# Optimization experiments

Measured on AMD Instinct MI355X. Metric: run time of the kernel, lower is better.

Reference implementation:

```python
import jax, jax.numpy as jnp
import numpy as np

N_NODES = 50000
N_EDGES = 800000
N_FEAT, N_HID, N_CLASS = 128, 128, 64


def _sage_conv(x, src, dst, Wl, Wr, b, n_nodes):
    # PyG SAGEConv (mean aggr): out = lin_l(mean_j x_j) + lin_r(x_i)
    msg = x[src]                                            # [E, d] gather
    agg = jax.ops.segment_sum(msg, dst, num_segments=n_nodes)
    deg = jax.ops.segment_sum(jnp.ones_like(dst, dtype=x.dtype), dst,
                              num_segments=n_nodes)
    agg = agg / jnp.maximum(deg, 1.0)[:, None]              # mean over in-neighbors
    return agg @ Wl + x @ Wr + b


def setup_inputs() -> dict:
    key = jax.random.key(0)
    ks = jax.random.split(key, 12)
    x = jax.random.normal(ks[0], (N_NODES, N_FEAT), dtype=jnp.float32)
    edge_index = jax.random.randint(ks[1], (2, N_EDGES), 0, N_NODES, dtype=jnp.int32)

    def glorot(k, fan_in, fan_out):
        s = jnp.sqrt(2.0 / (fan_in + fan_out)).astype(jnp.float32)
        return jax.random.normal(k, (fan_in, fan_out), dtype=jnp.float32) * s

    return {
        "x": x,
        "edge_index": edge_index,
        # layer 0: n_feat -> n_hid
        "Wl0": glorot(ks[2], N_FEAT, N_HID),
        "Wr0": glorot(ks[3], N_FEAT, N_HID),
        "b0": jnp.zeros((N_HID,), dtype=jnp.float32),
        # layer 1 (mid): n_hid -> n_hid
        "Wl1": glorot(ks[4], N_HID, N_HID),
        "Wr1": glorot(ks[5], N_HID, N_HID),
        "b1": jnp.zeros((N_HID,), dtype=jnp.float32),
        # layer 2 (out): n_hid -> n_class
        "Wl2": glorot(ks[6], N_HID, N_CLASS),
        "Wr2": glorot(ks[7], N_HID, N_CLASS),
        "b2": jnp.zeros((N_CLASS,), dtype=jnp.float32),
    }


def reference(x, edge_index, Wl0, Wr0, b0, Wl1, Wr1, b1, Wl2, Wr2, b2):
    src, dst = edge_index[0], edge_index[1]
    n = x.shape[0]
    # in_conv -> relu -> dropout(eval: identity)
    h = jax.nn.relu(_sage_conv(x, src, dst, Wl0, Wr0, b0, n))
    # mid_conv -> relu -> dropout(eval: identity)
    h = jax.nn.relu(_sage_conv(h, src, dst, Wl1, Wr1, b1, n))
    # out_conv (no relu/dropout)
    return _sage_conv(h, src, dst, Wl2, Wr2, b2, n)
```

## Files before the change

kernel.cpp:

```cpp
#include <hip/hip_runtime.h>

#define NFEAT 128
#define RS 128

using bf16x8 = __attribute__((ext_vector_type(8))) short;
using f32x4  = __attribute__((ext_vector_type(4))) float;
using f32x2  = __attribute__((ext_vector_type(2))) float;

__device__ __forceinline__ float bf2f(unsigned short u) {
    union { unsigned int i; float f; } v; v.i = ((unsigned int)u) << 16; return v.f;
}
__device__ __forceinline__ float bfhi2f(unsigned int hi16) {
    union { unsigned int i; float f; } v; v.i = hi16; return v.f;
}
__device__ __forceinline__ unsigned short f2bf(float f) {
    union { float f; unsigned int i; } v; v.f = f;
    unsigned int i = v.i;
    return (unsigned short)((i + 0x7FFFu + ((i >> 16) & 1u)) >> 16);
}
__device__ __forceinline__ unsigned int f4_to_fp8x4(float f0, float f1, float f2, float f3) {
    int p = __builtin_amdgcn_cvt_pk_fp8_f32(f0, f1, 0, false);
    p     = __builtin_amdgcn_cvt_pk_fp8_f32(f2, f3, p, true);
    return (unsigned int)p;
}


__global__ void zero_kernel(int* __restrict__ p, int n) {
    int i = blockIdx.x * 256 + threadIdx.x;
    if (i < n) p[i] = 0;
}

__global__ void hist_kernel(const int* __restrict__ dst, int* __restrict__ cnt,
                            int nE, int sliceN) {
    const int slice = blockIdx.x & 7;
    const int lo = slice * sliceN, hi = lo + sliceN;
    const int nb = gridDim.x >> 3;
    const int bs = blockIdx.x >> 3;
    for (int i = bs * 256 + threadIdx.x; i < nE; i += nb * 256) {
        int d = dst[i];
        if (d >= lo && d < hi) atomicAdd(&cnt[d], 1);
    }
}

__global__ void fill_kernel(const int* __restrict__ src, const int* __restrict__ dst,
                            int* __restrict__ cnt, int* __restrict__ col_idx,
                            int nE, int sliceN) {
    const int slice = blockIdx.x & 7;
    const int lo = slice * sliceN, hi = lo + sliceN;
    const int nb = gridDim.x >> 3;
    const int bs = blockIdx.x >> 3;
    for (int i = bs * 256 + threadIdx.x; i < nE; i += nb * 256) {
        int d = dst[i];
        int s = src[i];
        if (d >= lo && d < hi) {
            int pos = atomicAdd(&cnt[d], 1);
            col_idx[pos] = s;
        }
    }
}

__global__ void blocksum_kernel(const int* __restrict__ cnt, int* __restrict__ blockSum, int n) {
    int i = blockIdx.x * 256 + threadIdx.x;
    int d = (i < n) ? cnt[i] : 0;
    int lane = threadIdx.x & 63, wid = threadIdx.x >> 6;
    __shared__ int ws[4];
    int v = d;
    for (int off = 32; off; off >>= 1) v += __shfl_down(v, off);
    if (lane == 0) ws[wid] = v;
    __syncthreads();
    if (threadIdx.x == 0) blockSum[blockIdx.x] = ws[0] + ws[1] + ws[2] + ws[3];
}

__global__ void scan_write_kernel(int* __restrict__ cnt, const int* __restrict__ blockSum,
                                  int* __restrict__ row_ptr, float* __restrict__ inv_deg,
                                  int n) {
    const int b = blockIdx.x, tid = threadIdx.x;
    const int lane = tid & 63, wid = tid >> 6;
    __shared__ int wsA[4];
    __shared__ int wsB[4];
    int v = (tid < b) ? blockSum[tid] : 0;
    for (int off = 32; off; off >>= 1) v += __shfl_down(v, off);
    if (lane == 0) wsA[wid] = v;
    int i = b * 256 + tid;
    int d = (i < n) ? cnt[i] : 0;
    int s = d;
    for (int off = 1; off < 64; off <<= 1) {
        int t = __shfl_up(s, off);
        if (lane >= off) s += t;
    }
    if (lane == 63) wsB[wid] = s;
    __syncthreads();
    int blockOff = wsA[0] + wsA[1] + wsA[2] + wsA[3];
    int wOff = 0;
    for (int w = 0; w < wid; ++w) wOff += wsB[w];
    int excl = blockOff + wOff + s - d;
    if (i < n) {
        row_ptr[i] = excl;
        cnt[i]     = excl;
        inv_deg[i] = 1.0f / (float)(d > 1 ? d : 1);
    }
    if (i == n) row_ptr[n] = excl;
}


__global__ void xconv_kernel(const float* __restrict__ x, unsigned short* __restrict__ xc,
                             unsigned char* __restrict__ xq, int n) {
    int i = blockIdx.x * 256 + threadIdx.x;
    if (i >= n * 32) return;
    int node = i >> 5, fb = (i & 31) * 4;
    float4 v = *(const float4*)(x + (size_t)node * NFEAT + fb);
    uint2 hw;
    hw.x = (unsigned int)f2bf(v.x) | ((unsigned int)f2bf(v.y) << 16);
    hw.y = (unsigned int)f2bf(v.z) | ((unsigned int)f2bf(v.w) << 16);
    *(uint2*)(xc + (size_t)node * RS + fb) = hw;
    *(unsigned int*)(xq + (size_t)node * NFEAT + fb) = f4_to_fp8x4(v.x, v.y, v.z, v.w);
}

__global__ void wconv_all_kernel(const float* __restrict__ Wl0, const float* __restrict__ Wr0,
                                 const float* __restrict__ Wl1, const float* __restrict__ Wr1,
                                 const float* __restrict__ Wl2, const float* __restrict__ Wr2,
                                 unsigned short* __restrict__ Wsz0,
                                 unsigned short* __restrict__ Wsz1,
                                 unsigned short* __restrict__ Wsz2) {
    int idx = blockIdx.x * 256 + threadIdx.x;
    const float* Wl; const float* Wr; unsigned short* Wsz; int nout; int li;
    if (idx < 32768)      { Wl = Wl0; Wr = Wr0; Wsz = Wsz0; nout = 128; li = idx; }
    else if (idx < 65536) { Wl = Wl1; Wr = Wr1; Wsz = Wsz1; nout = 128; li = idx - 32768; }
    else if (idx < 81920) { Wl = Wl2; Wr = Wr2; Wsz = Wsz2; nout = 64;  li = idx - 65536; }
    else return;
    int c = li >> 8, k = li & 255;
    float f = (k < 128) ? Wl[k * nout + c] : Wr[(k - 128) * nout + c];
    Wsz[c * 256 + (k ^ ((c & 7) << 3))] = f2bf(f);
}

__global__ void agg_kernel(const unsigned char* __restrict__ xq,
                           const int* __restrict__ row_ptr, const int* __restrict__ col_idx,
                           const float* __restrict__ inv_deg,
                           unsigned short* __restrict__ agg, int n) {
    int lane = threadIdx.x & 7;
    int node = blockIdx.x * 32 + (threadIdx.x >> 3);
    if (node >= n) return;
    int beg = row_ptr[node], end = row_ptr[node + 1];
    float a[4][16];
    #pragma unroll
    for (int u = 0; u < 4; ++u)
        #pragma unroll
        for (int j = 0; j < 16; ++j) a[u][j] = 0.f;
    auto acc16 = [&](float* A, uint4 v) {
        f32x2 d;
        d = __builtin_amdgcn_cvt_pk_f32_fp8(v.x, false); A[0]  += d[0]; A[1]  += d[1];
        d = __builtin_amdgcn_cvt_pk_f32_fp8(v.x, true);  A[2]  += d[0]; A[3]  += d[1];
        d = __builtin_amdgcn_cvt_pk_f32_fp8(v.y, false); A[4]  += d[0]; A[5]  += d[1];
        d = __builtin_amdgcn_cvt_pk_f32_fp8(v.y, true);  A[6]  += d[0]; A[7]  += d[1];
        d = __builtin_amdgcn_cvt_pk_f32_fp8(v.z, false); A[8]  += d[0]; A[9]  += d[1];
        d = __builtin_amdgcn_cvt_pk_f32_fp8(v.z, true);  A[10] += d[0]; A[11] += d[1];
        d = __builtin_amdgcn_cvt_pk_f32_fp8(v.w, false); A[12] += d[0]; A[13] += d[1];
        d = __builtin_amdgcn_cvt_pk_f32_fp8(v.w, true);  A[14] += d[0]; A[15] += d[1];
    };
    int e = beg;
    for (; e + 8 <= end; e += 8) {
        uint4 v[8];
        #pragma unroll
        for (int u = 0; u < 8; ++u) {
            int s = col_idx[e + u];
            v[u] = *(const uint4*)(xq + (size_t)s * NFEAT + lane * 16);
        }
        #pragma unroll
        for (int u = 0; u < 8; ++u) acc16(a[u & 3], v[u]);
    }
    for (; e < end; ++e) {
        int s = col_idx[e];
        uint4 v = *(const uint4*)(xq + (size_t)s * NFEAT + lane * 16);
        acc16(a[0], v);
    }
    float sc = inv_deg[node];
    unsigned short hs[16];
    #pragma unroll
    for (int j = 0; j < 16; ++j)
        hs[j] = f2bf(((a[0][j] + a[1][j]) + (a[2][j] + a[3][j])) * sc);
    uint4 h0, h1;
    h0.x = (unsigned int)hs[0]  | ((unsigned int)hs[1]  << 16);
    h0.y = (unsigned int)hs[2]  | ((unsigned int)hs[3]  << 16);
    h0.z = (unsigned int)hs[4]  | ((unsigned int)hs[5]  << 16);
    h0.w = (unsigned int)hs[6]  | ((unsigned int)hs[7]  << 16);
    h1.x = (unsigned int)hs[8]  | ((unsigned int)hs[9]  << 16);
    h1.y = (unsigned int)hs[10] | ((unsigned int)hs[11] << 16);
    h1.z = (unsigned int)hs[12] | ((unsigned int)hs[13] << 16);
    h1.w = (unsigned int)hs[14] | ((unsigned int)hs[15] << 16);
    *(uint4*)(agg + (size_t)node * RS + lane * 16)     = h0;
    *(uint4*)(agg + (size_t)node * RS + lane * 16 + 8) = h1;
}


template<int NOUT, bool RELU, bool FINAL>
__global__ __launch_bounds__(256, 3) void mfma_gemm(
    const unsigned short* __restrict__ aggc, const unsigned short* __restrict__ xc,
    const unsigned short* __restrict__ Wsz, const float* __restrict__ bias,
    float* __restrict__ outF, unsigned short* __restrict__ outC,
    unsigned char* __restrict__ outQ, int n, int nRowTiles)
{
    __shared__ char smem[32768];
    const int tid  = threadIdx.x;
    const int wid  = tid >> 6, lane = tid & 63;
    const int rowTileI = blockIdx.x % nRowTiles;
    const int colTile  = (blockIdx.x / nRowTiles) * 64;

    {
        const char* wsrc = (const char*)(Wsz + (size_t)colTile * 256);
        #pragma unroll
        for (int i = 0; i < 8; ++i) {
            const int off = i * 4096 + wid * 1024;
            __builtin_amdgcn_global_load_lds(
                (const __attribute__((address_space(1))) unsigned int*)(wsrc + off + lane * 16),
                (__attribute__((address_space(3))) unsigned int*)(smem + off),
                16, 0, 0);
        }
    }

    const int lrow = lane & 15;
    const int lk   = (lane >> 4) * 8;
    const int lkb  = (lane >> 4) * 16;

    const int rowBase = rowTileI * 128 + wid * 32;
    int r0 = rowBase + lrow;      if (r0 > n - 1) r0 = n - 1;
    int r1 = rowBase + 16 + lrow; if (r1 > n - 1) r1 = n - 1;

    const unsigned short* Ar0 = aggc + (size_t)r0 * RS;
    const unsigned short* Ar1 = aggc + (size_t)r1 * RS;
    const unsigned short* Xr0 = xc   + (size_t)r0 * RS;
    const unsigned short* Xr1 = xc   + (size_t)r1 * RS;

    bf16x8 p0[2], p1[2];
    auto loadA = [&](int ks, int slot) {
        const unsigned short* P0 = (ks < 4) ? Ar0 : Xr0;
        const unsigned short* P1 = (ks < 4) ? Ar1 : Xr1;
        const int kk = (ks & 3) * 32 + lk;
        p0[slot] = *(const bf16x8*)(P0 + kk);
        p1[slot] = *(const bf16x8*)(P1 + kk);
    };
    loadA(0, 0);
    loadA(1, 1);

    int cbase[4], xmask[4];
    #pragma unroll
    for (int nf = 0; nf < 4; ++nf) {
        int cc = nf * 16 + lrow;
        cbase[nf] = (cc << 9) + lkb;
        xmask[nf] = (cc & 7) << 4;
    }

    __syncthreads();

    f32x4 acc[2][4];
    #pragma unroll
    for (int mf = 0; mf < 2; ++mf)
        #pragma unroll
        for (int nf = 0; nf < 4; ++nf)
            acc[mf][nf] = (f32x4){0.f, 0.f, 0.f, 0.f};

    bf16x8 b0 = *(const bf16x8*)(smem + (cbase[0] ^ xmask[0]));
    bf16x8 b1 = *(const bf16x8*)(smem + (cbase[1] ^ xmask[1]));
    bf16x8 b2 = *(const bf16x8*)(smem + (cbase[2] ^ xmask[2]));
    bf16x8 b3 = *(const bf16x8*)(smem + (cbase[3] ^ xmask[3]));

    #pragma unroll
    for (int ks = 0; ks < 8; ++ks) {
        const int slot = ks & 1;
        const bf16x8 c0 = p0[slot], c1 = p1[slot];
        const bf16x8 d0 = b0, d1 = b1, d2 = b2, d3 = b3;
        if (ks < 6) loadA(ks + 2, slot);
        if (ks < 7) {
            const int ko = (ks + 1) << 6;
            b0 = *(const bf16x8*)(smem + ((cbase[0] + ko) ^ xmask[0]));
            b1 = *(const bf16x8*)(smem + ((cbase[1] + ko) ^ xmask[1]));
            b2 = *(const bf16x8*)(smem + ((cbase[2] + ko) ^ xmask[2]));
            b3 = *(const bf16x8*)(smem + ((cbase[3] + ko) ^ xmask[3]));
        }
        acc[0][0] = __builtin_amdgcn_mfma_f32_16x16x32_bf16(c0, d0, acc[0][0], 0, 0, 0);
        acc[1][0] = __builtin_amdgcn_mfma_f32_16x16x32_bf16(c1, d0, acc[1][0], 0, 0, 0);
        acc[0][1] = __builtin_amdgcn_mfma_f32_16x16x32_bf16(c0, d1, acc[0][1], 0, 0, 0);
        acc[1][1] = __builtin_amdgcn_mfma_f32_16x16x32_bf16(c1, d1, acc[1][1], 0, 0, 0);
        acc[0][2] = __builtin_amdgcn_mfma_f32_16x16x32_bf16(c0, d2, acc[0][2], 0, 0, 0);
        acc[1][2] = __builtin_amdgcn_mfma_f32_16x16x32_bf16(c1, d2, acc[1][2], 0, 0, 0);
        acc[0][3] = __builtin_amdgcn_mfma_f32_16x16x32_bf16(c0, d3, acc[0][3], 0, 0, 0);
        acc[1][3] = __builtin_amdgcn_mfma_f32_16x16x32_bf16(c1, d3, acc[1][3], 0, 0, 0);
    }

    #pragma unroll
    for (int mf = 0; mf < 2; ++mf) {
        #pragma unroll
        for (int nf = 0; nf < 4; ++nf) {
            const int c = colTile + nf * 16 + lrow;
            const float bv = bias[c];
            #pragma unroll
            for (int reg = 0; reg < 4; ++reg) {
                const int r = rowBase + mf * 16 + (lane >> 4) * 4 + reg;
                if (r < n) {
                    float h = acc[mf][nf][reg] + bv;
                    if (RELU) h = fmaxf(h, 0.f);
                    if (FINAL) {
                        outF[(size_t)r * NOUT + c] = h;
                    } else {
                        outC[(size_t)r * RS + c] = f2bf(h);
                        outQ[(size_t)r * NFEAT + c] =
                            (unsigned char)(__builtin_amdgcn_cvt_pk_fp8_f32(h, h, 0, false) & 0xFF);
                    }
                }
            }
        }
    }
}

extern "C" void kernel_launch(void* const* d_in, const int* in_sizes, int n_in,
                              void* d_out, int out_size, void* d_ws, size_t ws_size,
                              hipStream_t stream) {
    const float* x   = (const float*)d_in[0];
    const int*   ei  = (const int*)d_in[1];
    const float* Wl0 = (const float*)d_in[2];
    const float* Wr0 = (const float*)d_in[3];
    const float* b0  = (const float*)d_in[4];
    const float* Wl1 = (const float*)d_in[5];
    const float* Wr1 = (const float*)d_in[6];
    const float* b1  = (const float*)d_in[7];
    const float* Wl2 = (const float*)d_in[8];
    const float* Wr2 = (const float*)d_in[9];
    const float* b2  = (const float*)d_in[10];

    const int nN = in_sizes[0] / NFEAT;
    const int nE = in_sizes[1] / 2;
    const int* src = ei;
    const int* dst = ei + nE;

    char* ws = (char*)d_ws;
    size_t off = 0;
    auto take = [&](size_t bytes) { char* p = ws + off; off += (bytes + 255) & ~(size_t)255; return p; };
    int*   cnt      = (int*)  take((size_t)nN * 4);
    int*   row_ptr  = (int*)  take((size_t)(nN + 1) * 4);
    int*   col_idx  = (int*)  take((size_t)nE * 4);
    float* inv_deg  = (float*)take((size_t)nN * 4);
    int*   blockSum = (int*)  take(256 * 4);
    const size_t plane  = (size_t)nN * RS * 2;
    const size_t qplane = (size_t)nN * NFEAT;
    unsigned short* aggC = (unsigned short*)take(plane);
    unsigned short* xc0  = (unsigned short*)take(plane);
    unsigned short* xc1  = (unsigned short*)take(plane);
    unsigned char*  xq0  = (unsigned char*) take(qplane);
    unsigned char*  xq1  = (unsigned char*) take(qplane);
    unsigned short* Wsz0 = (unsigned short*)take(128 * 256 * 2);
    unsigned short* Wsz1 = (unsigned short*)take(128 * 256 * 2);
    unsigned short* Wsz2 = (unsigned short*)take(64 * 256 * 2);
    (void)ws_size; (void)n_in; (void)out_size;

    const int scanBlocks = (nN + 255) / 256;
    const int sliceN = (nN + 7) / 8;

    zero_kernel<<<scanBlocks, 256, 0, stream>>>(cnt, nN);
    hist_kernel<<<2048, 256, 0, stream>>>(dst, cnt, nE, sliceN);
    blocksum_kernel<<<scanBlocks, 256, 0, stream>>>(cnt, blockSum, nN);
    scan_write_kernel<<<scanBlocks, 256, 0, stream>>>(cnt, blockSum, row_ptr, inv_deg, nN);
    fill_kernel<<<2048, 256, 0, stream>>>(src, dst, cnt, col_idx, nE, sliceN);

    xconv_kernel<<<(nN * 32 + 255) / 256, 256, 0, stream>>>(x, xc0, xq0, nN);
    wconv_all_kernel<<<(81920 + 255) / 256, 256, 0, stream>>>(
        Wl0, Wr0, Wl1, Wr1, Wl2, Wr2, Wsz0, Wsz1, Wsz2);

    const int aggGrid   = (nN + 31) / 32;
    const int nRowTiles = (nN + 127) / 128;
    const int gBig = nRowTiles * 2;
    const int gFin = nRowTiles;

    agg_kernel<<<aggGrid, 256, 0, stream>>>(xq0, row_ptr, col_idx, inv_deg, aggC, nN);
    mfma_gemm<128, true, false><<<gBig, 256, 0, stream>>>(
        aggC, xc0, Wsz0, b0, nullptr, xc1, xq1, nN, nRowTiles);
    agg_kernel<<<aggGrid, 256, 0, stream>>>(xq1, row_ptr, col_idx, inv_deg, aggC, nN);
    mfma_gemm<128, true, false><<<gBig, 256, 0, stream>>>(
        aggC, xc1, Wsz1, b1, nullptr, xc0, xq0, nN, nRowTiles);
    agg_kernel<<<aggGrid, 256, 0, stream>>>(xq0, row_ptr, col_idx, inv_deg, aggC, nN);
    mfma_gemm<64, false, true><<<gFin, 256, 0, stream>>>(
        aggC, xc0, Wsz2, b2, (float*)d_out, nullptr, nullptr, nN, nRowTiles);
}
```

Before: 215.7 us.

## Fuse neighbor aggregation into per-layer MFMA GEMM kernel and merge prep kernels

```diff
diff --git a/kernel.cpp b/kernel.cpp
--- a/kernel.cpp
+++ b/kernel.cpp
@@ -24,11 +24,6 @@
     return (unsigned int)p;
 }
 
-
-__global__ void zero_kernel(int* __restrict__ p, int n) {
-    int i = blockIdx.x * 256 + threadIdx.x;
-    if (i < n) p[i] = 0;
-}
 
 __global__ void hist_kernel(const int* __restrict__ dst, int* __restrict__ cnt,
                             int nE, int sliceN) {
@@ -103,115 +98,67 @@
 }
 
 
-__global__ void xconv_kernel(const float* __restrict__ x, unsigned short* __restrict__ xc,
-                             unsigned char* __restrict__ xq, int n) {
-    int i = blockIdx.x * 256 + threadIdx.x;
-    if (i >= n * 32) return;
-    int node = i >> 5, fb = (i & 31) * 4;
-    float4 v = *(const float4*)(x + (size_t)node * NFEAT + fb);
-    uint2 hw;
-    hw.x = (unsigned int)f2bf(v.x) | ((unsigned int)f2bf(v.y) << 16);
-    hw.y = (unsigned int)f2bf(v.z) | ((unsigned int)f2bf(v.w) << 16);
-    *(uint2*)(xc + (size_t)node * RS + fb) = hw;
-    *(unsigned int*)(xq + (size_t)node * NFEAT + fb) = f4_to_fp8x4(v.x, v.y, v.z, v.w);
-}
-
-__global__ void wconv_all_kernel(const float* __restrict__ Wl0, const float* __restrict__ Wr0,
-                                 const float* __restrict__ Wl1, const float* __restrict__ Wr1,
-                                 const float* __restrict__ Wl2, const float* __restrict__ Wr2,
-                                 unsigned short* __restrict__ Wsz0,
-                                 unsigned short* __restrict__ Wsz1,
-                                 unsigned short* __restrict__ Wsz2) {
+__global__ void prep_kernel(const float* __restrict__ x,
+                            unsigned short* __restrict__ xc, unsigned char* __restrict__ xq,
+                            const float* __restrict__ Wl0, const float* __restrict__ Wr0,
+                            const float* __restrict__ Wl1, const float* __restrict__ Wr1,
+                            const float* __restrict__ Wl2, const float* __restrict__ Wr2,
+                            unsigned short* __restrict__ Wsz0,
+                            unsigned short* __restrict__ Wsz1,
+                            unsigned short* __restrict__ Wsz2,
+                            int* __restrict__ cnt, int n) {
     int idx = blockIdx.x * 256 + threadIdx.x;
-    const float* Wl; const float* Wr; unsigned short* Wsz; int nout; int li;
-    if (idx < 32768)      { Wl = Wl0; Wr = Wr0; Wsz = Wsz0; nout = 128; li = idx; }
-    else if (idx < 65536) { Wl = Wl1; Wr = Wr1; Wsz = Wsz1; nout = 128; li = idx - 32768; }
-    else if (idx < 81920) { Wl = Wl2; Wr = Wr2; Wsz = Wsz2; nout = 64;  li = idx - 65536; }
-    else return;
-    int c = li >> 8, k = li & 255;
-    float f = (k < 128) ? Wl[k * nout + c] : Wr[(k - 128) * nout + c];
-    Wsz[c * 256 + (k ^ ((c & 7) << 3))] = f2bf(f);
-}
-
-__global__ void agg_kernel(const unsigned char* __restrict__ xq,
-                           const int* __restrict__ row_ptr, const int* __restrict__ col_idx,
-                           const float* __restrict__ inv_deg,
-                           unsigned short* __restrict__ agg, int n) {
-    int lane = threadIdx.x & 7;
-    int node = blockIdx.x * 32 + (threadIdx.x >> 3);
-    if (node >= n) return;
-    int beg = row_ptr[node], end = row_ptr[node + 1];
-    float a[4][16];
-    #pragma unroll
-    for (int u = 0; u < 4; ++u)
-        #pragma unroll
-        for (int j = 0; j < 16; ++j) a[u][j] = 0.f;
-    auto acc16 = [&](float* A, uint4 v) {
-        f32x2 d;
-        d = __builtin_amdgcn_cvt_pk_f32_fp8(v.x, false); A[0]  += d[0]; A[1]  += d[1];
-        d = __builtin_amdgcn_cvt_pk_f32_fp8(v.x, true);  A[2]  += d[0]; A[3]  += d[1];
-        d = __builtin_amdgcn_cvt_pk_f32_fp8(v.y, false); A[4]  += d[0]; A[5]  += d[1];
-        d = __builtin_amdgcn_cvt_pk_f32_fp8(v.y, true);  A[6]  += d[0]; A[7]  += d[1];
-        d = __builtin_amdgcn_cvt_pk_f32_fp8(v.z, false); A[8]  += d[0]; A[9]  += d[1];
-        d = __builtin_amdgcn_cvt_pk_f32_fp8(v.z, true);  A[10] += d[0]; A[11] += d[1];
-        d = __builtin_amdgcn_cvt_pk_f32_fp8(v.w, false); A[12] += d[0]; A[13] += d[1];
-        d = __builtin_amdgcn_cvt_pk_f32_fp8(v.w, true);  A[14] += d[0]; A[15] += d[1];
-    };
-    int e = beg;
-    for (; e + 8 <= end; e += 8) {
-        uint4 v[8];
-        #pragma unroll
-        for (int u = 0; u < 8; ++u) {
-            int s = col_idx[e + u];
-            v[u] = *(const uint4*)(xq + (size_t)s * NFEAT + lane * 16);
-        }
-        #pragma unroll
-        for (int u = 0; u < 8; ++u) acc16(a[u & 3], v[u]);
-    }
-    for (; e < end; ++e) {
-        int s = col_idx[e];
-        uint4 v = *(const uint4*)(xq + (size_t)s * NFEAT + lane * 16);
-        acc16(a[0], v);
-    }
-    float sc = inv_deg[node];
-    unsigned short hs[16];
-    #pragma unroll
-    for (int j = 0; j < 16; ++j)
-        hs[j] = f2bf(((a[0][j] + a[1][j]) + (a[2][j] + a[3][j])) * sc);
-    uint4 h0, h1;
-    h0.x = (unsigned int)hs[0]  | ((unsigned int)hs[1]  << 16);
-    h0.y = (unsigned int)hs[2]  | ((unsigned int)hs[3]  << 16);
-    h0.z = (unsigned int)hs[4]  | ((unsigned int)hs[5]  << 16);
-    h0.w = (unsigned int)hs[6]  | ((unsigned int)hs[7]  << 16);
-    h1.x = (unsigned int)hs[8]  | ((unsigned int)hs[9]  << 16);
-    h1.y = (unsigned int)hs[10] | ((unsigned int)hs[11] << 16);
-    h1.z = (unsigned int)hs[12] | ((unsigned int)hs[13] << 16);
-    h1.w = (unsigned int)hs[14] | ((unsigned int)hs[15] << 16);
-    *(uint4*)(agg + (size_t)node * RS + lane * 16)     = h0;
-    *(uint4*)(agg + (size_t)node * RS + lane * 16 + 8) = h1;
+    const int R0 = n * 32;
+    if (idx < R0) {
+        int node = idx >> 5, fb = (idx & 31) * 4;
+        float4 v = *(const float4*)(x + (size_t)node * NFEAT + fb);
+        uint2 hw;
+        hw.x = (unsigned int)f2bf(v.x) | ((unsigned int)f2bf(v.y) << 16);
+        hw.y = (unsigned int)f2bf(v.z) | ((unsigned int)f2bf(v.w) << 16);
+        *(uint2*)(xc + (size_t)node * RS + fb) = hw;
+        *(unsigned int*)(xq + (size_t)node * NFEAT + fb) = f4_to_fp8x4(v.x, v.y, v.z, v.w);
+        return;
+    }
+    idx -= R0;
+    if (idx < 81920) {
+        const float* Wl; const float* Wr; unsigned short* Wsz; int nout; int li;
+        if (idx < 32768)      { Wl = Wl0; Wr = Wr0; Wsz = Wsz0; nout = 128; li = idx; }
+        else if (idx < 65536) { Wl = Wl1; Wr = Wr1; Wsz = Wsz1; nout = 128; li = idx - 32768; }
+        else                  { Wl = Wl2; Wr = Wr2; Wsz = Wsz2; nout = 64;  li = idx - 65536; }
+        int c = li >> 8, k = li & 255;
+        float f = (k < 128) ? Wl[k * nout + c] : Wr[(k - 128) * nout + c];
+        Wsz[c * 256 + (k ^ ((c & 7) << 3))] = f2bf(f);
+        return;
+    }
+    idx -= 81920;
+    if (idx < n) cnt[idx] = 0;
 }
 
 
 template<int NOUT, bool RELU, bool FINAL>
-__global__ __launch_bounds__(256, 3) void mfma_gemm(
-    const unsigned short* __restrict__ aggc, const unsigned short* __restrict__ xc,
+__global__ __launch_bounds__(512, 4) void layer_kernel(
+    const unsigned char* __restrict__ xq, const unsigned short* __restrict__ xc,
+    const int* __restrict__ row_ptr, const int* __restrict__ col_idx,
+    const float* __restrict__ inv_deg,
     const unsigned short* __restrict__ Wsz, const float* __restrict__ bias,
     float* __restrict__ outF, unsigned short* __restrict__ outC,
-    unsigned char* __restrict__ outQ, int n, int nRowTiles)
+    unsigned char* __restrict__ outQ, int n)
 {
-    __shared__ char smem[32768];
+    constexpr int HALVES = NOUT / 64;
+    constexpr int AOFF = 32768;
+    __shared__ char smem[32768 + 16384];
     const int tid  = threadIdx.x;
-    const int wid  = tid >> 6, lane = tid & 63;
-    const int rowTileI = blockIdx.x % nRowTiles;
-    const int colTile  = (blockIdx.x / nRowTiles) * 64;
+    const int lane = tid & 63;
+    const int wid  = tid >> 6;
+    const int rowBase = blockIdx.x * 64;
 
     {
-        const char* wsrc = (const char*)(Wsz + (size_t)colTile * 256);
+        const char* wsrc = (const char*)Wsz;
         #pragma unroll
-        for (int i = 0; i < 8; ++i) {
-            const int off = i * 4096 + wid * 1024;
+        for (int i = 0; i < 4; ++i) {
+            const int off = (i * 512 + tid) * 16;
             __builtin_amdgcn_global_load_lds(
-                (const __attribute__((address_space(1))) unsigned int*)(wsrc + off + lane * 16),
+                (const __attribute__((address_space(1))) unsigned int*)(wsrc + off),
                 (__attribute__((address_space(3))) unsigned int*)(smem + off),
                 16, 0, 0);
         }
@@ -219,91 +166,133 @@
 
     const int lrow = lane & 15;
     const int lk   = (lane >> 4) * 8;
-    const int lkb  = (lane >> 4) * 16;
-
-    const int rowBase = rowTileI * 128 + wid * 32;
-    int r0 = rowBase + lrow;      if (r0 > n - 1) r0 = n - 1;
-    int r1 = rowBase + 16 + lrow; if (r1 > n - 1) r1 = n - 1;
-
-    const unsigned short* Ar0 = aggc + (size_t)r0 * RS;
-    const unsigned short* Ar1 = aggc + (size_t)r1 * RS;
-    const unsigned short* Xr0 = xc   + (size_t)r0 * RS;
-    const unsigned short* Xr1 = xc   + (size_t)r1 * RS;
-
-    bf16x8 p0[2], p1[2];
-    auto loadA = [&](int ks, int slot) {
-        const unsigned short* P0 = (ks < 4) ? Ar0 : Xr0;
-        const unsigned short* P1 = (ks < 4) ? Ar1 : Xr1;
-        const int kk = (ks & 3) * 32 + lk;
-        p0[slot] = *(const bf16x8*)(P0 + kk);
-        p1[slot] = *(const bf16x8*)(P1 + kk);
-    };
-    loadA(0, 0);
-    loadA(1, 1);
-
-    int cbase[4], xmask[4];
+    const int rg   = wid >> 1;
+    const int cg   = wid & 1;
+    int r0 = rowBase + rg * 16 + lrow; if (r0 > n - 1) r0 = n - 1;
+    const unsigned short* Xr = xc + (size_t)r0 * RS;
+    bf16x8 xr[4];
     #pragma unroll
-    for (int nf = 0; nf < 4; ++nf) {
-        int cc = nf * 16 + lrow;
-        cbase[nf] = (cc << 9) + lkb;
-        xmask[nf] = (cc & 7) << 4;
+    for (int ks = 0; ks < 4; ++ks) xr[ks] = *(const bf16x8*)(Xr + ks * 32 + lk);
+    __builtin_amdgcn_sched_barrier(0);
+
+    {
+        const int l    = tid & 7;
+        const int nd   = tid >> 3;
+        const int node = rowBase + nd;
+        if (node < n) {
+            int beg = row_ptr[node], end = row_ptr[node + 1];
+            float a[2][16];
+            #pragma unroll
+            for (int u = 0; u < 2; ++u)
+                #pragma unroll
+                for (int j = 0; j < 16; ++j) a[u][j] = 0.f;
+            auto acc16 = [&](float* A, uint4 v) {
+                f32x2 d;
+                d = __builtin_amdgcn_cvt_pk_f32_fp8(v.x, false); A[0]  += d[0]; A[1]  += d[1];
+                d = __builtin_amdgcn_cvt_pk_f32_fp8(v.x, true);  A[2]  += d[0]; A[3]  += d[1];
+                d = __builtin_amdgcn_cvt_pk_f32_fp8(v.y, false); A[4]  += d[0]; A[5]  += d[1];
+                d = __builtin_amdgcn_cvt_pk_f32_fp8(v.y, true);  A[6]  += d[0]; A[7]  += d[1];
+                d = __builtin_amdgcn_cvt_pk_f32_fp8(v.z, false); A[8]  += d[0]; A[9]  += d[1];
+                d = __builtin_amdgcn_cvt_pk_f32_fp8(v.z, true);  A[10] += d[0]; A[11] += d[1];
+                d = __builtin_amdgcn_cvt_pk_f32_fp8(v.w, false); A[12] += d[0]; A[13] += d[1];
+                d = __builtin_amdgcn_cvt_pk_f32_fp8(v.w, true);  A[14] += d[0]; A[15] += d[1];
+            };
+            int e = beg;
+            for (; e + 8 <= end; e += 8) {
+                uint4 v[8];
+                #pragma unroll
+                for (int u = 0; u < 8; ++u) {
+                    int s = col_idx[e + u];
+                    v[u] = *(const uint4*)(xq + (size_t)s * NFEAT + l * 16);
+                }
+                #pragma unroll
+                for (int u = 0; u < 8; ++u) acc16(a[u & 1], v[u]);
+            }
+            for (; e < end; ++e) {
+                int s = col_idx[e];
+                uint4 v = *(const uint4*)(xq + (size_t)s * NFEAT + l * 16);
+                acc16(a[0], v);
+            }
+            float sc = inv_deg[node];
+            unsigned short hs[16];
+            #pragma unroll
+            for (int j = 0; j < 16; ++j)
+                hs[j] = f2bf((a[0][j] + a[1][j]) * sc);
+            uint4 h0, h1;
+            h0.x = (unsigned int)hs[0]  | ((unsigned int)hs[1]  << 16);
+            h0.y = (unsigned int)hs[2]  | ((unsigned int)hs[3]  << 16);
+            h0.z = (unsigned int)hs[4]  | ((unsigned int)hs[5]  << 16);
+            h0.w = (unsigned int)hs[6]  | ((unsigned int)hs[7]  << 16);
+            h1.x = (unsigned int)hs[8]  | ((unsigned int)hs[9]  << 16);
+            h1.y = (unsigned int)hs[10] | ((unsigned int)hs[11] << 16);
+            h1.z = (unsigned int)hs[12] | ((unsigned int)hs[13] << 16);
+            h1.w = (unsigned int)hs[14] | ((unsigned int)hs[15] << 16);
+            const int s_ = nd & 7;
+            char* arow = smem + AOFF + nd * 256;
+            *(uint4*)(arow + (((2 * l)     ^ s_) << 4)) = h0;
+            *(uint4*)(arow + (((2 * l + 1) ^ s_) << 4)) = h1;
+        }
     }
 
     __syncthreads();
 
-    f32x4 acc[2][4];
+    const int cc0 = cg * 32 + lrow;
+    const int cc1 = cg * 32 + 16 + lrow;
+    const int cb0 = (cc0 << 9) + ((lane >> 4) * 16), xm0 = (cc0 & 7) << 4;
+    const int cb1 = (cc1 << 9) + ((lane >> 4) * 16), xm1 = (cc1 & 7) << 4;
+    const int ar    = rg * 16 + lrow;
+    const int abase = AOFF + ar * 256;
+    const int as    = ar & 7;
+
     #pragma unroll
-    for (int mf = 0; mf < 2; ++mf)
+    for (int h = 0; h < HALVES; ++h) {
+        if (h > 0) {
+            __syncthreads();
+            const char* wsrc = (const char*)(Wsz + (size_t)h * 64 * 256);
+            #pragma unroll
+            for (int i = 0; i < 4; ++i) {
+                const int off = (i * 512 + tid) * 16;
+                __builtin_amdgcn_global_load_lds(
+                    (const __attribute__((address_space(1))) unsigned int*)(wsrc + off),
+                    (__attribute__((address_space(3))) unsigned int*)(smem + off),
+                    16, 0, 0);
+            }
+            __syncthreads();
+        }
+
+        f32x4 acc0 = (f32x4){0.f, 0.f, 0.f, 0.f};
+        f32x4 acc1 = (f32x4){0.f, 0.f, 0.f, 0.f};
+
         #pragma unroll
-        for (int nf = 0; nf < 4; ++nf)
-            acc[mf][nf] = (f32x4){0.f, 0.f, 0.f, 0.f};
-
-    bf16x8 b0 = *(const bf16x8*)(smem + (cbase[0] ^ xmask[0]));
-    bf16x8 b1 = *(const bf16x8*)(smem + (cbase[1] ^ xmask[1]));
-    bf16x8 b2 = *(const bf16x8*)(smem + (cbase[2] ^ xmask[2]));
-    bf16x8 b3 = *(const bf16x8*)(smem + (cbase[3] ^ xmask[3]));
-
-    #pragma unroll
-    for (int ks = 0; ks < 8; ++ks) {
-        const int slot = ks & 1;
-        const bf16x8 c0 = p0[slot], c1 = p1[slot];
-        const bf16x8 d0 = b0, d1 = b1, d2 = b2, d3 = b3;
-        if (ks < 6) loadA(ks + 2, slot);
-        if (ks < 7) {
-            const int ko = (ks + 1) << 6;
-            b0 = *(const bf16x8*)(smem + ((cbase[0] + ko) ^ xmask[0]));
-            b1 = *(const bf16x8*)(smem + ((cbase[1] + ko) ^ xmask[1]));
-            b2 = *(const bf16x8*)(smem + ((cbase[2] + ko) ^ xmask[2]));
-            b3 = *(const bf16x8*)(smem + ((cbase[3] + ko) ^ xmask[3]));
-        }
-        acc[0][0] = __builtin_amdgcn_mfma_f32_16x16x32_bf16(c0, d0, acc[0][0], 0, 0, 0);
-        acc[1][0] = __builtin_amdgcn_mfma_f32_16x16x32_bf16(c1, d0, acc[1][0], 0, 0, 0);
-        acc[0][1] = __builtin_amdgcn_mfma_f32_16x16x32_bf16(c0, d1, acc[0][1], 0, 0, 0);
-        acc[1][1] = __builtin_amdgcn_mfma_f32_16x16x32_bf16(c1, d1, acc[1][1], 0, 0, 0);
-        acc[0][2] = __builtin_amdgcn_mfma_f32_16x16x32_bf16(c0, d2, acc[0][2], 0, 0, 0);
-        acc[1][2] = __builtin_amdgcn_mfma_f32_16x16x32_bf16(c1, d2, acc[1][2], 0, 0, 0);
-        acc[0][3] = __builtin_amdgcn_mfma_f32_16x16x32_bf16(c0, d3, acc[0][3], 0, 0, 0);
-        acc[1][3] = __builtin_amdgcn_mfma_f32_16x16x32_bf16(c1, d3, acc[1][3], 0, 0, 0);
-    }
-
-    #pragma unroll
-    for (int mf = 0; mf < 2; ++mf) {
+        for (int ks = 0; ks < 8; ++ks) {
+            bf16x8 a;
+            if (ks < 4)
+                a = *(const bf16x8*)(smem + abase + (((ks * 4 + (lane >> 4)) ^ as) << 4));
+            else
+                a = xr[ks - 4];
+            bf16x8 b0 = *(const bf16x8*)(smem + ((cb0 + (ks << 6)) ^ xm0));
+            bf16x8 b1 = *(const bf16x8*)(smem + ((cb1 + (ks << 6)) ^ xm1));
+            acc0 = __builtin_amdgcn_mfma_f32_16x16x32_bf16(a, b0, acc0, 0, 0, 0);
+            acc1 = __builtin_amdgcn_mfma_f32_16x16x32_bf16(a, b1, acc1, 0, 0, 0);
+        }
+
         #pragma unroll
-        for (int nf = 0; nf < 4; ++nf) {
-            const int c = colTile + nf * 16 + lrow;
+        for (int nf = 0; nf < 2; ++nf) {
+            const f32x4 av = nf ? acc1 : acc0;
+            const int c = h * 64 + cg * 32 + nf * 16 + lrow;
             const float bv = bias[c];
             #pragma unroll
             for (int reg = 0; reg < 4; ++reg) {
-                const int r = rowBase + mf * 16 + (lane >> 4) * 4 + reg;
+                const int r = rowBase + rg * 16 + (lane >> 4) * 4 + reg;
                 if (r < n) {
-                    float h = acc[mf][nf][reg] + bv;
-                    if (RELU) h = fmaxf(h, 0.f);
+                    float hv = av[reg] + bv;
+                    if (RELU) hv = fmaxf(hv, 0.f);
                     if (FINAL) {
-                        outF[(size_t)r * NOUT + c] = h;
+                        outF[(size_t)r * NOUT + c] = hv;
                     } else {
-                        outC[(size_t)r * RS + c] = f2bf(h);
+                        outC[(size_t)r * RS + c] = f2bf(hv);
                         outQ[(size_t)r * NFEAT + c] =
-                            (unsigned char)(__builtin_amdgcn_cvt_pk_fp8_f32(h, h, 0, false) & 0xFF);
+                            (unsigned char)(__builtin_amdgcn_cvt_pk_fp8_f32(hv, hv, 0, false) & 0xFF);
                     }
                 }
             }
@@ -341,7 +330,6 @@
     int*   blockSum = (int*)  take(256 * 4);
     const size_t plane  = (size_t)nN * RS * 2;
     const size_t qplane = (size_t)nN * NFEAT;
-    unsigned short* aggC = (unsigned short*)take(plane);
     unsigned short* xc0  = (unsigned short*)take(plane);
     unsigned short* xc1  = (unsigned short*)take(plane);
     unsigned char*  xq0  = (unsigned char*) take(qplane);
@@ -354,28 +342,21 @@
     const int scanBlocks = (nN + 255) / 256;
     const int sliceN = (nN + 7) / 8;
 
-    zero_kernel<<<scanBlocks, 256, 0, stream>>>(cnt, nN);
+    const int prepTotal = nN * 32 + 81920 + nN;
+    prep_kernel<<<(prepTotal + 255) / 256, 256, 0, stream>>>(
+        x, xc0, xq0, Wl0, Wr0, Wl1, Wr1, Wl2, Wr2, Wsz0, Wsz1, Wsz2, cnt, nN);
+
     hist_kernel<<<2048, 256, 0, stream>>>(dst, cnt, nE, sliceN);
     blocksum_kernel<<<scanBlocks, 256, 0, stream>>>(cnt, blockSum, nN);
     scan_write_kernel<<<scanBlocks, 256, 0, stream>>>(cnt, blockSum, row_ptr, inv_deg, nN);
     fill_kernel<<<2048, 256, 0, stream>>>(src, dst, cnt, col_idx, nE, sliceN);
 
-    xconv_kernel<<<(nN * 32 + 255) / 256, 256, 0, stream>>>(x, xc0, xq0, nN);
-    wconv_all_kernel<<<(81920 + 255) / 256, 256, 0, stream>>>(
-        Wl0, Wr0, Wl1, Wr1, Wl2, Wr2, Wsz0, Wsz1, Wsz2);
-
-    const int aggGrid   = (nN + 31) / 32;
-    const int nRowTiles = (nN + 127) / 128;
-    const int gBig = nRowTiles * 2;
-    const int gFin = nRowTiles;
-
-    agg_kernel<<<aggGrid, 256, 0, stream>>>(xq0, row_ptr, col_idx, inv_deg, aggC, nN);
-    mfma_gemm<128, true, false><<<gBig, 256, 0, stream>>>(
-        aggC, xc0, Wsz0, b0, nullptr, xc1, xq1, nN, nRowTiles);
-    agg_kernel<<<aggGrid, 256, 0, stream>>>(xq1, row_ptr, col_idx, inv_deg, aggC, nN);
-    mfma_gemm<128, true, false><<<gBig, 256, 0, stream>>>(
-        aggC, xc1, Wsz1, b1, nullptr, xc0, xq0, nN, nRowTiles);
-    agg_kernel<<<aggGrid, 256, 0, stream>>>(xq0, row_ptr, col_idx, inv_deg, aggC, nN);
-    mfma_gemm<64, false, true><<<gFin, 256, 0, stream>>>(
-        aggC, xc0, Wsz2, b2, (float*)d_out, nullptr, nullptr, nN, nRowTiles);
-}
+    const int layerGrid = (nN + 63) / 64;
+
+    layer_kernel<128, true, false><<<layerGrid, 512, 0, stream>>>(
+        xq0, xc0, row_ptr, col_idx, inv_deg, Wsz0, b0, nullptr, xc1, xq1, nN);
+    layer_kernel<128, true, false><<<layerGrid, 512, 0, stream>>>(
+        xq1, xc1, row_ptr, col_idx, inv_deg, Wsz1, b1, nullptr, xc0, xq0, nN);
+    layer_kernel<64, false, true><<<layerGrid, 512, 0, stream>>>(
+        xq0, xc0, row_ptr, col_idx, inv_deg, Wsz2, b2, (float*)d_out, nullptr, nullptr, nN);
+}
```

Result: faster. 205.6 us (-4.7%).
